# Optimization experiments

Hardware: AMD Instinct MI355X
Metric: run time of the kernel (lower is better)

## Reference

```python
import jax, jax.numpy as jnp
import numpy as np

NUM_HEADS = 12
WS = 8
ROPE_BASE = 100.0  # croco/dust3r RoPE2D default frequency base


def _rope1d(t, p, inv_freq):
    # t: [Bw, h, N, d], p: [Bw, N], inv_freq: [d/2]
    freqs = p[..., None] * inv_freq                      # [Bw, N, d/2]
    emb = jnp.concatenate([freqs, freqs], axis=-1)       # [Bw, N, d]
    cos = jnp.cos(emb)[:, None, :, :]
    sin = jnp.sin(emb)[:, None, :, :]
    t1, t2 = jnp.split(t, 2, axis=-1)
    rot = jnp.concatenate([-t2, t1], axis=-1)            # rotate_half
    return t * cos + rot * sin


def _rope2d(tokens, pos):
    # tokens: [Bw, h, N, D], pos: [Bw, N, 2] (y, x). First D/2 dims use y, last D/2 use x.
    D = tokens.shape[-1]
    d = D // 2
    inv_freq = 1.0 / (ROPE_BASE ** (jnp.arange(0, d, 2, dtype=jnp.float32) / d))
    ty, tx = jnp.split(tokens, 2, axis=-1)
    return jnp.concatenate([_rope1d(ty, pos[..., 0], inv_freq),
                            _rope1d(tx, pos[..., 1], inv_freq)], axis=-1)


def setup_inputs() -> dict:
    B, H, W, C = 16, 64, 64, 768
    key = jax.random.key(0)
    ks = jax.random.split(key, 7)
    x_img = jax.random.normal(ks[0], (B, H * W, C), dtype=jnp.float32)
    yy, xx = jnp.meshgrid(jnp.arange(H), jnp.arange(W), indexing='ij')
    pos = jnp.stack([yy, xx], axis=-1).reshape(1, H * W, 2).astype(jnp.float32)
    pos2d_img = jnp.broadcast_to(pos, (B, H * W, 2))
    unseen = jax.random.normal(ks[1], (B, C), dtype=jnp.float32)
    sc = C ** -0.5
    qkv_w = jax.random.normal(ks[2], (3 * C, C), dtype=jnp.float32) * sc
    qkv_b = jax.random.normal(ks[3], (3 * C,), dtype=jnp.float32) * 0.02
    proj_w = jax.random.normal(ks[4], (C, C), dtype=jnp.float32) * sc
    proj_b = jax.random.normal(ks[5], (C,), dtype=jnp.float32) * 0.02
    return {'x_img': x_img, 'pos2d_img': pos2d_img, 'unseen': unseen,
            'qkv_w': qkv_w, 'qkv_b': qkv_b, 'proj_w': proj_w, 'proj_b': proj_b,
            'H': H, 'W': W}


def reference(x_img, pos2d_img, unseen, qkv_w, qkv_b, proj_w, proj_b, H, W):
    B, HW, C = x_img.shape
    hd = C // NUM_HEADS
    scale = hd ** -0.5
    nWh, nWw = H // WS, W // WS
    Bwin, Nwin = B * nWh * nWw, WS * WS

    # window partition
    xw = x_img.reshape(B, nWh, WS, nWw, WS, C).transpose(0, 1, 3, 2, 4, 5).reshape(Bwin, Nwin, C)
    pw = pos2d_img.reshape(B, nWh, WS, nWw, WS, 2).transpose(0, 1, 3, 2, 4, 5).reshape(Bwin, Nwin, 2)

    # append unseen token (shared across windows of an image)
    u = jnp.broadcast_to(unseen[:, None, None, :], (B, nWh * nWw, 1, C)).reshape(Bwin, 1, C)
    xw = jnp.concatenate([xw, u], axis=1)                # [Bwin, Nwin+1, C]

    qkv = xw @ qkv_w.T + qkv_b                           # [Bwin, N, 3C]
    qkv = qkv.reshape(Bwin, Nwin + 1, 3, NUM_HEADS, hd)
    q = qkv[:, :, 0].transpose(0, 2, 1, 3)               # [Bwin, h, N, hd]
    k = qkv[:, :, 1].transpose(0, 2, 1, 3)
    v = qkv[:, :, 2].transpose(0, 2, 1, 3)

    # RoPE2D on image tokens only; unseen token gets no RoPE
    q = jnp.concatenate([_rope2d(q[:, :, :Nwin], pw), q[:, :, Nwin:]], axis=2)
    k = jnp.concatenate([_rope2d(k[:, :, :Nwin], pw), k[:, :, Nwin:]], axis=2)

    attn = jax.nn.softmax(jnp.einsum('bhqd,bhkd->bhqk', q, k) * scale, axis=-1)
    out = jnp.einsum('bhqk,bhkd->bhqd', attn, v)
    out = out.transpose(0, 2, 1, 3).reshape(Bwin, Nwin + 1, C)
    out = out @ proj_w.T + proj_b

    # window merge
    out_img = out[:, :Nwin].reshape(B, nWh, nWw, WS, WS, C).transpose(0, 1, 3, 2, 4, 5).reshape(B, HW, C)
    out_unseen = out[:, Nwin].reshape(B, nWh * nWw, C).mean(axis=1)  # [B, C]
    return out_img, out_unseen
```

## Files before the change

### kernel.cpp

```cpp
#include <hip/hip_runtime.h>
#include <cstdint>
#include <cstddef>

typedef __attribute__((ext_vector_type(8)))  __bf16 bf16x8;
typedef __attribute__((ext_vector_type(4)))  float  f32x4;
typedef __attribute__((ext_vector_type(2)))  unsigned int u32x2;
typedef __attribute__((ext_vector_type(4)))  unsigned int u32x4;

#define DI __device__ __forceinline__

constexpr int Cdim = 768;
constexpr int C3   = 2304;
constexpr int NT   = 65;
constexpr int ROWS = 1024 * NT;
constexpr int ROWS_PAD = ROWS + 32;
constexpr int TP   = 96;
constexpr int PS   = 128;
constexpr long long OUT_IMG = 16LL * 4096 * 768;

DI float bf2f(unsigned short u) { unsigned int x = (unsigned int)u << 16; float f; __builtin_memcpy(&f, &x, 4); return f; }
DI unsigned short f2bf(float f) { unsigned int x; __builtin_memcpy(&x, &f, 4); x = x + 0x7fffu + ((x >> 16) & 1u); return (unsigned short)(x >> 16); }

DI void gload_lds16(const unsigned short* g, unsigned short* l) {
  __builtin_amdgcn_global_load_lds((__attribute__((address_space(1))) void*)g,
                                   (__attribute__((address_space(3))) void*)l, 16, 0, 0);
}

__global__ void k_prep(const float* __restrict__ qkv_w, const float* __restrict__ proj_w,
                       unsigned short* __restrict__ wqb, unsigned short* __restrict__ wpb,
                       float* __restrict__ rope) {
  const int NW1 = 2304 * 768;
  const int NW2 = 768 * 768;
  int total = NW1 + NW2 + 1024;
  for (int i = blockIdx.x * blockDim.x + threadIdx.x; i < total; i += gridDim.x * blockDim.x) {
    if (i < NW1) wqb[i] = f2bf(qkv_w[i]);
    else if (i < NW1 + NW2) wpb[i - NW1] = f2bf(proj_w[i - NW1]);
    else {
      int e = i - NW1 - NW2;
      int p = e >> 4, j = e & 15;
      float inv = powf(100.f, -(float)j * (1.f / 16.f));
      float a = (float)p * inv;
      rope[2 * e]     = cosf(a);
      rope[2 * e + 1] = sinf(a);
    }
  }
}

__global__ void k_xw(const float* __restrict__ x, const float* __restrict__ unseen,
                     unsigned short* __restrict__ xw) {
  int row = blockIdx.x;
  int w = row / NT, t = row - w * NT;
  const float* src;
  if (t == 64) {
    src = unseen + (size_t)(w >> 6) * Cdim;
  } else {
    int wy = (w >> 3) & 7, wx = w & 7;
    int hw = ((wy << 3) + (t >> 3)) * 64 + (wx << 3) + (t & 7);
    src = x + ((size_t)(w >> 6) * 4096 + hw) * Cdim;
  }
  float4 v = ((const float4*)src)[threadIdx.x];
  unsigned int u0 = (unsigned)f2bf(v.x) | ((unsigned)f2bf(v.y) << 16);
  unsigned int u1 = (unsigned)f2bf(v.z) | ((unsigned)f2bf(v.w) << 16);
  ((u32x2*)(xw + (size_t)row * Cdim))[threadIdx.x] = (u32x2){u0, u1};
}

template<int MODE, int NTILES>
__global__ __launch_bounds__(256, 4) void k_gemm(
    const unsigned short* __restrict__ A, const unsigned short* __restrict__ Bw,
    const float* __restrict__ bias, const float* __restrict__ rope,
    unsigned short* __restrict__ Cb, float* __restrict__ outp) {
  constexpr int K = 768;
  __shared__ alignas(16) unsigned short As[128 * 64];
  __shared__ alignas(16) unsigned short Bs[128 * 64];

  constexpr int nwg = 520 * NTILES;
  constexpr int q8 = nwg / 8, r8 = nwg % 8;
  int id = blockIdx.x;
  int xcd = id & 7, lid = id >> 3;
  int wg = (xcd < r8 ? xcd * (q8 + 1) : r8 * (q8 + 1) + (xcd - r8) * q8) + lid;
  int mtile = wg / NTILES, ntile = wg - mtile * NTILES;
  int m0 = mtile * 128, n0 = ntile * 128;

  int tid = threadIdx.x;
  int lane = tid & 63, wid = tid >> 6;
  int lq = lane & 15, lg = lane >> 4;
  int wm = (wid >> 1) * 64;
  int wn = (wid & 1) * 64;

  f32x4 acc[4][4];
  #pragma unroll
  for (int i = 0; i < 4; ++i)
    #pragma unroll
    for (int j = 0; j < 4; ++j) acc[i][j] = (f32x4){0.f, 0.f, 0.f, 0.f};

  for (int kt = 0; kt < K / 64; ++kt) {
    int k0 = kt * 64;
    #pragma unroll
    for (int c = 0; c < 4; ++c) {
      int chunk = c * 256 + tid;
      int row = chunk >> 3, kc = chunk & 7;
      int skc = kc ^ (row & 7);
      gload_lds16(A + (size_t)(m0 + row) * K + k0 + skc * 8,
                  As + (size_t)(c * 256 + (tid & ~63)) * 8);
    }
    #pragma unroll
    for (int c = 0; c < 4; ++c) {
      int chunk = c * 256 + tid;
      int row = chunk >> 3, kc = chunk & 7;
      int skc = kc ^ (row & 7);
      gload_lds16(Bw + (size_t)(n0 + row) * K + k0 + skc * 8,
                  Bs + (size_t)(c * 256 + (tid & ~63)) * 8);
    }
    asm volatile("s_waitcnt vmcnt(0)" ::: "memory");
    __syncthreads();
    #pragma unroll
    for (int ks = 0; ks < 2; ++ks) {
      bf16x8 af[4], bfr[4];
      #pragma unroll
      for (int mt = 0; mt < 4; ++mt) {
        int row = wm + mt * 16 + lq;
        int ch = ((ks << 2) + lg) ^ (row & 7);
        af[mt] = *(const bf16x8*)(As + row * 64 + ch * 8);
      }
      #pragma unroll
      for (int nt = 0; nt < 4; ++nt) {
        int row = wn + nt * 16 + lq;
        int ch = ((ks << 2) + lg) ^ (row & 7);
        bfr[nt] = *(const bf16x8*)(Bs + row * 64 + ch * 8);
      }
      #pragma unroll
      for (int mt = 0; mt < 4; ++mt)
        #pragma unroll
        for (int nt = 0; nt < 4; ++nt)
          acc[mt][nt] = __builtin_amdgcn_mfma_f32_16x16x32_bf16(af[mt], bfr[nt], acc[mt][nt], 0, 0, 0);
    }
    __syncthreads();
  }

  if (MODE == 0) {
    unsigned short* ct = As;
    #pragma unroll
    for (int mt = 0; mt < 4; ++mt) {
      #pragma unroll
      for (int r = 0; r < 4; ++r) {
        int lrow = wm + mt * 16 + (lg << 2) + r;
        int grow = m0 + lrow;
        int w = grow / NT, t = grow - w * NT;
        int wy = (w >> 3) & 7, wx = w & 7;
        int py = (wy << 3) + (t >> 3), px = (wx << 3) + (t & 7);
        #pragma unroll
        for (int a = 0; a < 2; ++a) {
          int cn0 = wn + a * 32 + lq;
          int col0 = n0 + cn0, col1 = col0 + 16;
          float v0 = acc[mt][2 * a][r] + bias[col0];
          float v1 = acc[mt][2 * a + 1][r] + bias[col1];
          if (col0 < 1536 && t != 64) {
            int p = a ? px : py;
            const float* rp = rope + ((p << 4) + lq) * 2;
            float cc = rp[0], ss = rp[1];
            float o0 = v0 * cc - v1 * ss;
            float o1 = v1 * cc + v0 * ss;
            v0 = o0; v1 = o1;
          }
          int b0 = (lrow * 256 + cn0 * 2) ^ ((lrow & 7) << 4);
          int b1 = (lrow * 256 + (cn0 + 16) * 2) ^ ((lrow & 7) << 4);
          *(unsigned short*)((char*)ct + b0) = f2bf(v0);
          *(unsigned short*)((char*)ct + b1) = f2bf(v1);
        }
      }
    }
    __syncthreads();
    #pragma unroll
    for (int j = 0; j < 8; ++j) {
      int idx = j * 256 + tid;
      int row = idx >> 4, c = idx & 15;
      u32x4 v = *(const u32x4*)((char*)ct + row * 256 + ((c ^ (row & 7)) << 4));
      *(u32x4*)(Cb + (size_t)(m0 + row) * C3 + n0 + c * 8) = v;
    }
  } else {
    float* cf = (float*)As;
    #pragma unroll
    for (int half = 0; half < 2; ++half) {
      if ((wm >> 6) == half) {
        #pragma unroll
        for (int mt = 0; mt < 4; ++mt) {
          #pragma unroll
          for (int r = 0; r < 4; ++r) {
            int lrow = mt * 16 + (lg << 2) + r;
            int grow = m0 + half * 64 + lrow;
            int w = grow / NT, t = grow - w * NT;
            #pragma unroll
            for (int a = 0; a < 2; ++a) {
              int cn0 = wn + a * 32 + lq;
              int col0 = n0 + cn0, col1 = col0 + 16;
              float v0 = acc[mt][2 * a][r] + bias[col0];
              float v1 = acc[mt][2 * a + 1][r] + bias[col1];
              if (t == 64) {
                float* ub = outp + OUT_IMG + (size_t)(w >> 6) * Cdim;
                atomicAdd(ub + col0, v0 * (1.f / 64.f));
                atomicAdd(ub + col1, v1 * (1.f / 64.f));
              } else {
                int b0 = (lrow * 512 + cn0 * 4) ^ ((lrow & 7) << 4);
                int b1 = (lrow * 512 + (cn0 + 16) * 4) ^ ((lrow & 7) << 4);
                *(float*)((char*)cf + b0) = v0;
                *(float*)((char*)cf + b1) = v1;
              }
            }
          }
        }
      }
      __syncthreads();
      #pragma unroll
      for (int j = 0; j < 8; ++j) {
        int idx = j * 256 + tid;
        int row = idx >> 5, c = idx & 31;
        int grow = m0 + half * 64 + row;
        int w = grow / NT, t = grow - w * NT;
        if (t != 64) {
          int wy = (w >> 3) & 7, wx = w & 7;
          int py = (wy << 3) + (t >> 3), px = (wx << 3) + (t & 7);
          u32x4 v = *(const u32x4*)((char*)cf + row * 512 + ((c ^ (row & 7)) << 4));
          *(u32x4*)(outp + ((size_t)(w >> 6) * 4096 + py * 64 + px) * Cdim + n0 + c * 4) = v;
        }
      }
      __syncthreads();
    }
  }
}

__global__ void k_vt(const unsigned short* __restrict__ qkv, unsigned short* __restrict__ Vt) {
  int bh = blockIdx.x;
  int w = bh / 12, h = bh - w * 12;
  __shared__ float sv[65][65];
  const unsigned short* base = qkv + (size_t)w * NT * C3 + 1536 + h * 64;
  for (int i = threadIdx.x; i < 65 * 64; i += 256) {
    int t = i >> 6, d = i & 63;
    sv[t][d] = bf2f(base[(size_t)t * C3 + d]);
  }
  __syncthreads();
  unsigned short* out = Vt + (size_t)bh * 64 * TP;
  for (int i = threadIdx.x; i < 64 * (TP / 8); i += 256) {
    int d = i / (TP / 8), tc = i - d * (TP / 8);
    int t0 = tc * 8;
    unsigned int u[4];
    #pragma unroll
    for (int k = 0; k < 4; ++k) {
      int ta = t0 + 2 * k, tb = ta + 1;
      unsigned short sa = (ta < 65) ? f2bf(sv[ta][d]) : (unsigned short)0;
      unsigned short sb = (tb < 65) ? f2bf(sv[tb][d]) : (unsigned short)0;
      u[k] = (unsigned)sa | ((unsigned)sb << 16);
    }
    *(u32x4*)(out + d * TP + t0) = (u32x4){u[0], u[1], u[2], u[3]};
  }
}

__global__ __launch_bounds__(64) void k_attn(const unsigned short* __restrict__ qkv,
                                             const unsigned short* __restrict__ Vt,
                                             unsigned short* __restrict__ att) {
  __shared__ alignas(16) unsigned short P[16 * PS];
  int h = blockIdx.x, w = blockIdx.y;
  int lane = threadIdx.x;
  int lq = lane & 15, lg = lane >> 4;

  const unsigned short* qb = qkv + (size_t)w * NT * C3 + h * 64;
  const unsigned short* kb = qb + 768;

  bf16x8 kf[5][2];
  #pragma unroll
  for (int kt = 0; kt < 5; ++kt)
    #pragma unroll
    for (int ks = 0; ks < 2; ++ks)
      kf[kt][ks] = *(const bf16x8*)(kb + (size_t)(kt * 16 + lq) * C3 + ks * 32 + lg * 8);

  const unsigned short* vb = Vt + (size_t)(w * 12 + h) * 64 * TP;
  bf16x8 vf[3][4];
  #pragma unroll
  for (int ks = 0; ks < 3; ++ks)
    #pragma unroll
    for (int dt = 0; dt < 4; ++dt)
      vf[ks][dt] = *(const bf16x8*)(vb + (size_t)(dt * 16 + lq) * TP + ks * 32 + lg * 8);

  for (int i = lane; i < 16 * 8; i += 64) {
    int row = i >> 3, j = i & 7;
    int byteo = (row * (PS * 2) + 160 + j * 4) ^ ((row & 7) << 4);
    *(unsigned int*)((char*)P + byteo) = 0u;
  }

  #pragma unroll 1
  for (int qt = 0; qt < 5; ++qt) {
    bf16x8 qf[2];
    #pragma unroll
    for (int ks = 0; ks < 2; ++ks)
      qf[ks] = *(const bf16x8*)(qb + (size_t)(qt * 16 + lq) * C3 + ks * 32 + lg * 8);

    f32x4 sa[5];
    #pragma unroll
    for (int kt = 0; kt < 5; ++kt) {
      sa[kt] = (f32x4){0.f, 0.f, 0.f, 0.f};
      #pragma unroll
      for (int ks = 0; ks < 2; ++ks)
        sa[kt] = __builtin_amdgcn_mfma_f32_16x16x32_bf16(kf[kt][ks], qf[ks], sa[kt], 0, 0, 0);
    }
    float pv[5][4];
    float m = -1e30f;
    #pragma unroll
    for (int kt = 0; kt < 5; ++kt)
      #pragma unroll
      for (int r = 0; r < 4; ++r) {
        int tok = kt * 16 + lg * 4 + r;
        float s = sa[kt][r] * 0.125f;
        bool ok = tok < 65;
        pv[kt][r] = ok ? s : -1e30f;
        m = (ok && s > m) ? s : m;
      }
    m = fmaxf(m, __shfl_xor(m, 16));
    m = fmaxf(m, __shfl_xor(m, 32));
    float sum = 0.f;
    #pragma unroll
    for (int kt = 0; kt < 5; ++kt)
      #pragma unroll
      for (int r = 0; r < 4; ++r) {
        float e = (pv[kt][r] > -1e29f) ? exp2f((pv[kt][r] - m) * 1.44269504f) : 0.f;
        pv[kt][r] = e;
        sum += e;
      }
    sum += __shfl_xor(sum, 16);
    sum += __shfl_xor(sum, 32);
    float rinv = 1.f / sum;

    int q = qt * 16 + lq;
    #pragma unroll
    for (int kt = 0; kt < 5; ++kt) {
      unsigned int u0 = (unsigned)f2bf(pv[kt][0] * rinv) | ((unsigned)f2bf(pv[kt][1] * rinv) << 16);
      unsigned int u1 = (unsigned)f2bf(pv[kt][2] * rinv) | ((unsigned)f2bf(pv[kt][3] * rinv) << 16);
      int byteo = (lq * (PS * 2) + kt * 32 + lg * 8) ^ ((lq & 7) << 4);
      *(u32x2*)((char*)P + byteo) = (u32x2){u0, u1};
    }
    asm volatile("s_waitcnt lgkmcnt(0)" ::: "memory");

    bf16x8 bp[3];
    #pragma unroll
    for (int ks = 0; ks < 3; ++ks) {
      int byteo = (lq * (PS * 2) + ks * 64 + lg * 16) ^ ((lq & 7) << 4);
      bp[ks] = *(const bf16x8*)((char*)P + byteo);
    }
    #pragma unroll
    for (int dt = 0; dt < 4; ++dt) {
      f32x4 o = (f32x4){0.f, 0.f, 0.f, 0.f};
      #pragma unroll
      for (int ks = 0; ks < 3; ++ks)
        o = __builtin_amdgcn_mfma_f32_16x16x32_bf16(vf[ks][dt], bp[ks], o, 0, 0, 0);
      if (q < 65) {
        unsigned int u0 = (unsigned)f2bf(o[0]) | ((unsigned)f2bf(o[1]) << 16);
        unsigned int u1 = (unsigned)f2bf(o[2]) | ((unsigned)f2bf(o[3]) << 16);
        *(u32x2*)(att + (size_t)(w * NT + q) * Cdim + h * 64 + dt * 16 + lg * 4) = (u32x2){u0, u1};
      }
    }
  }
}

extern "C" void kernel_launch(void* const* d_in, const int* in_sizes, int n_in,
                              void* d_out, int out_size, void* d_ws, size_t ws_size,
                              hipStream_t stream) {
  const float* x_img  = (const float*)d_in[0];
  const float* unseen = (const float*)d_in[2];
  const float* qkv_w  = (const float*)d_in[3];
  const float* qkv_b  = (const float*)d_in[4];
  const float* proj_w = (const float*)d_in[5];
  const float* proj_b = (const float*)d_in[6];

  char* ws = (char*)d_ws;
  size_t off = 0;
  auto alloc = [&](size_t bytes) { void* p = ws + off; off = (off + bytes + 255) & ~(size_t)255; return p; };
  unsigned short* xw  = (unsigned short*)alloc((size_t)ROWS * Cdim * 2);
  unsigned short* qkv = (unsigned short*)alloc((size_t)ROWS_PAD * C3 * 2);
  unsigned short* Vt  = (unsigned short*)alloc((size_t)12288 * 64 * TP * 2);
  unsigned short* wqb = (unsigned short*)alloc((size_t)C3 * Cdim * 2);
  unsigned short* wpb = (unsigned short*)alloc((size_t)Cdim * Cdim * 2);
  float* rope = (float*)alloc(64 * 16 * 2 * sizeof(float));

  hipMemsetAsync((float*)d_out + OUT_IMG, 0, 16 * Cdim * sizeof(float), stream);

  k_prep<<<512, 256, 0, stream>>>(qkv_w, proj_w, wqb, wpb, rope);
  k_xw<<<ROWS, 192, 0, stream>>>(x_img, unseen, xw);
  k_gemm<0, 18><<<520 * 18, 256, 0, stream>>>(xw, wqb, qkv_b, rope, qkv, nullptr);
  k_vt<<<12288, 256, 0, stream>>>(qkv, Vt);
  k_attn<<<dim3(12, 1024), 64, 0, stream>>>(qkv, Vt, xw);
  k_gemm<1, 6><<<520 * 6, 256, 0, stream>>>(xw, wpb, proj_b, nullptr, nullptr, (float*)d_out);
}
```

Baseline: 657.2 us.

## Fuse V transpose into attention kernel and handle 65th key separately

Removes the separate k_vt kernel, which read V from the qkv buffer and wrote a padded transposed copy to global memory. Each attention block now stages its 64 V rows in shared memory and builds the transposed MFMA operands from there. The 65th (unseen) key is handled with a scalar rank-1 update instead of a third padded MFMA k-step, which also removes the zero-padding of P. This saves a kernel launch and a global round trip of V, at the cost of strided 2-byte LDS reads and extra shuffles inside the attention kernel.

```diff
diff --git a/kernel.cpp b/kernel.cpp
--- a/kernel.cpp
+++ b/kernel.cpp
@@ -14,7 +14,6 @@
 constexpr int NT   = 65;
 constexpr int ROWS = 1024 * NT;
 constexpr int ROWS_PAD = ROWS + 32;
-constexpr int TP   = 96;
 constexpr int PS   = 128;
 constexpr long long OUT_IMG = 16LL * 4096 * 768;
 
@@ -228,42 +227,27 @@
   }
 }
 
-__global__ void k_vt(const unsigned short* __restrict__ qkv, unsigned short* __restrict__ Vt) {
-  int bh = blockIdx.x;
-  int w = bh / 12, h = bh - w * 12;
-  __shared__ float sv[65][65];
-  const unsigned short* base = qkv + (size_t)w * NT * C3 + 1536 + h * 64;
-  for (int i = threadIdx.x; i < 65 * 64; i += 256) {
-    int t = i >> 6, d = i & 63;
-    sv[t][d] = bf2f(base[(size_t)t * C3 + d]);
-  }
-  __syncthreads();
-  unsigned short* out = Vt + (size_t)bh * 64 * TP;
-  for (int i = threadIdx.x; i < 64 * (TP / 8); i += 256) {
-    int d = i / (TP / 8), tc = i - d * (TP / 8);
-    int t0 = tc * 8;
-    unsigned int u[4];
-    #pragma unroll
-    for (int k = 0; k < 4; ++k) {
-      int ta = t0 + 2 * k, tb = ta + 1;
-      unsigned short sa = (ta < 65) ? f2bf(sv[ta][d]) : (unsigned short)0;
-      unsigned short sb = (tb < 65) ? f2bf(sv[tb][d]) : (unsigned short)0;
-      u[k] = (unsigned)sa | ((unsigned)sb << 16);
-    }
-    *(u32x4*)(out + d * TP + t0) = (u32x4){u[0], u[1], u[2], u[3]};
-  }
-}
-
 __global__ __launch_bounds__(64) void k_attn(const unsigned short* __restrict__ qkv,
-                                             const unsigned short* __restrict__ Vt,
                                              unsigned short* __restrict__ att) {
   __shared__ alignas(16) unsigned short P[16 * PS];
+  __shared__ alignas(16) unsigned short Vs[64 * 68];
   int h = blockIdx.x, w = blockIdx.y;
   int lane = threadIdx.x;
   int lq = lane & 15, lg = lane >> 4;
 
   const unsigned short* qb = qkv + (size_t)w * NT * C3 + h * 64;
   const unsigned short* kb = qb + 768;
+  const unsigned short* vsrc = qb + 1536;
+
+  {
+    int ts = lane >> 3, c = lane & 7;
+    #pragma unroll
+    for (int j = 0; j < 8; ++j) {
+      int tt = j * 8 + ts;
+      u32x4 v = *(const u32x4*)(vsrc + (size_t)tt * C3 + c * 8);
+      *(u32x4*)(Vs + tt * 68 + c * 8) = v;
+    }
+  }
 
   bf16x8 kf[5][2];
   #pragma unroll
@@ -272,19 +256,30 @@
     for (int ks = 0; ks < 2; ++ks)
       kf[kt][ks] = *(const bf16x8*)(kb + (size_t)(kt * 16 + lq) * C3 + ks * 32 + lg * 8);
 
-  const unsigned short* vb = Vt + (size_t)(w * 12 + h) * 64 * TP;
-  bf16x8 vf[3][4];
+  const unsigned short* v64p = vsrc + (size_t)64 * C3;
+  float v64f[4][4];
   #pragma unroll
-  for (int ks = 0; ks < 3; ++ks)
-    #pragma unroll
-    for (int dt = 0; dt < 4; ++dt)
-      vf[ks][dt] = *(const bf16x8*)(vb + (size_t)(dt * 16 + lq) * TP + ks * 32 + lg * 8);
-
-  for (int i = lane; i < 16 * 8; i += 64) {
-    int row = i >> 3, j = i & 7;
-    int byteo = (row * (PS * 2) + 160 + j * 4) ^ ((row & 7) << 4);
-    *(unsigned int*)((char*)P + byteo) = 0u;
-  }
+  for (int dt = 0; dt < 4; ++dt) {
+    u32x2 u = *(const u32x2*)(v64p + dt * 16 + lg * 4);
+    v64f[dt][0] = bf2f((unsigned short)(u[0] & 0xffff));
+    v64f[dt][1] = bf2f((unsigned short)(u[0] >> 16));
+    v64f[dt][2] = bf2f((unsigned short)(u[1] & 0xffff));
+    v64f[dt][3] = bf2f((unsigned short)(u[1] >> 16));
+  }
+
+  bf16x8 vf[2][4];
+  #pragma unroll
+  for (int ks = 0; ks < 2; ++ks)
+    #pragma unroll
+    for (int dt = 0; dt < 4; ++dt) {
+      int d = dt * 16 + lq;
+      int t0 = ks * 32 + lg * 8;
+      bf16x8 v;
+      #pragma unroll
+      for (int j = 0; j < 8; ++j)
+        v[j] = *(const __bf16*)(Vs + (t0 + j) * 68 + d);
+      vf[ks][dt] = v;
+    }
 
   #pragma unroll 1
   for (int qt = 0; qt < 5; ++qt) {
@@ -330,17 +325,19 @@
 
     int q = qt * 16 + lq;
     #pragma unroll
-    for (int kt = 0; kt < 5; ++kt) {
+    for (int kt = 0; kt < 4; ++kt) {
       unsigned int u0 = (unsigned)f2bf(pv[kt][0] * rinv) | ((unsigned)f2bf(pv[kt][1] * rinv) << 16);
       unsigned int u1 = (unsigned)f2bf(pv[kt][2] * rinv) | ((unsigned)f2bf(pv[kt][3] * rinv) << 16);
       int byteo = (lq * (PS * 2) + kt * 32 + lg * 8) ^ ((lq & 7) << 4);
       *(u32x2*)((char*)P + byteo) = (u32x2){u0, u1};
     }
+    float p64 = pv[4][0] * rinv;
+    p64 = __shfl(p64, lq);
     asm volatile("s_waitcnt lgkmcnt(0)" ::: "memory");
 
-    bf16x8 bp[3];
-    #pragma unroll
-    for (int ks = 0; ks < 3; ++ks) {
+    bf16x8 bp[2];
+    #pragma unroll
+    for (int ks = 0; ks < 2; ++ks) {
       int byteo = (lq * (PS * 2) + ks * 64 + lg * 16) ^ ((lq & 7) << 4);
       bp[ks] = *(const bf16x8*)((char*)P + byteo);
     }
@@ -348,8 +345,10 @@
     for (int dt = 0; dt < 4; ++dt) {
       f32x4 o = (f32x4){0.f, 0.f, 0.f, 0.f};
       #pragma unroll
-      for (int ks = 0; ks < 3; ++ks)
+      for (int ks = 0; ks < 2; ++ks)
         o = __builtin_amdgcn_mfma_f32_16x16x32_bf16(vf[ks][dt], bp[ks], o, 0, 0, 0);
+      #pragma unroll
+      for (int r = 0; r < 4; ++r) o[r] += p64 * v64f[dt][r];
       if (q < 65) {
         unsigned int u0 = (unsigned)f2bf(o[0]) | ((unsigned)f2bf(o[1]) << 16);
         unsigned int u1 = (unsigned)f2bf(o[2]) | ((unsigned)f2bf(o[3]) << 16);
@@ -374,7 +373,6 @@
   auto alloc = [&](size_t bytes) { void* p = ws + off; off = (off + bytes + 255) & ~(size_t)255; return p; };
   unsigned short* xw  = (unsigned short*)alloc((size_t)ROWS * Cdim * 2);
   unsigned short* qkv = (unsigned short*)alloc((size_t)ROWS_PAD * C3 * 2);
-  unsigned short* Vt  = (unsigned short*)alloc((size_t)12288 * 64 * TP * 2);
   unsigned short* wqb = (unsigned short*)alloc((size_t)C3 * Cdim * 2);
   unsigned short* wpb = (unsigned short*)alloc((size_t)Cdim * Cdim * 2);
   float* rope = (float*)alloc(64 * 16 * 2 * sizeof(float));
@@ -384,7 +382,6 @@
   k_prep<<<512, 256, 0, stream>>>(qkv_w, proj_w, wqb, wpb, rope);
   k_xw<<<ROWS, 192, 0, stream>>>(x_img, unseen, xw);
   k_gemm<0, 18><<<520 * 18, 256, 0, stream>>>(xw, wqb, qkv_b, rope, qkv, nullptr);
-  k_vt<<<12288, 256, 0, stream>>>(qkv, Vt);
-  k_attn<<<dim3(12, 1024), 64, 0, stream>>>(qkv, Vt, xw);
+  k_attn<<<dim3(12, 1024), 64, 0, stream>>>(qkv, xw);
   k_gemm<1, 6><<<520 * 6, 256, 0, stream>>>(xw, wpb, proj_b, nullptr, nullptr, (float*)d_out);
 }
```

Result: faster. 595.2 us (median of 2 runs) (-9.4%).
